# Kernel tuning notes

Measured on AMD Instinct MI355X. Metric: run time of the kernel, lower is better.

## Reference

```python
import jax, jax.numpy as jnp
import numpy as np

N_BATCH = 50000   # nodes being aggregated (rows of mask)
N_UNIQUE = 100000 # unique neighbor nodes (cols of mask / rows of features)
K = 16            # sampled neighbors per node
HID = 256
POOL = 128


def setup_inputs() -> dict:
    key = jax.random.key(0)
    k1, k2, k3 = jax.random.split(key, 3)
    neigh_idx = jax.random.randint(k1, (N_BATCH, K), 0, N_UNIQUE, dtype=jnp.int64)
    features = jax.random.normal(k2, (N_UNIQUE, HID), dtype=jnp.float32)
    # pool_layer weight, nn.Linear(hid, pool, bias=False): shape [pool, hid]
    W = jax.random.normal(k3, (POOL, HID), dtype=jnp.float32) * (1.0 / np.sqrt(HID))
    return {"neigh_idx": neigh_idx, "features": features, "W": W}


def reference(neigh_idx, features, W):
    # pool_feats = pool_layer(features): [M, POOL]
    pool_feats = jnp.einsum("mh,ph->mp", features, W)
    # mean over sampled neighbors, equivalent to (mask / num_neigh) @ pool_feats
    # without materializing the dense [N, M] mask.
    to_feats = jnp.mean(pool_feats[neigh_idx], axis=1)  # [N, POOL]
    return to_feats
```

## Files before the change

kernel.cpp:

```cpp
#include <hip/hip_runtime.h>


#define N_NODES  50000
#define N_UNIQUE 100000
#define KNEI     16
#define HID      256
#define POOL     128

#define NBLOCKS  512
#define NPB      ((N_NODES + NBLOCKS - 1) / NBLOCKS)

__global__ __launch_bounds__(256) void fused_meanpool_kernel(
    const int*   __restrict__ idx,
    const float* __restrict__ feats,
    const float* __restrict__ W,
    float* __restrict__ out)
{
    __shared__ float  mf[HID];
    __shared__ float4 part[8][32];

    const int tid = threadIdx.x;
    const int og  = tid & 31;
    const int ksl = tid >> 5;

    float4 w[4][8];
#pragma unroll
    for (int e = 0; e < 4; ++e) {
        const float* wr = W + (size_t)(og * 4 + e) * HID + ksl * 32;
#pragma unroll
        for (int j4 = 0; j4 < 8; ++j4)
            w[e][j4] = *reinterpret_cast<const float4*>(wr + j4 * 4);
    }

    const int node0 = blockIdx.x * NPB;
    for (int i = 0; i < NPB; ++i) {
        const int node = node0 + i;
        if (node >= N_NODES) break;

        const int* ip = idx + node * KNEI;
        float v = 0.f;
#pragma unroll
        for (int k = 0; k < KNEI; ++k) {
            int r = ip[k];
            r = ((unsigned)r < (unsigned)N_UNIQUE) ? r : 0;
            v += feats[(size_t)r * HID + tid];
        }
        mf[tid] = v;
        __syncthreads();

        float4 acc = make_float4(0.f, 0.f, 0.f, 0.f);
        const float4* mfp = reinterpret_cast<const float4*>(&mf[ksl * 32]);
#pragma unroll
        for (int j4 = 0; j4 < 8; ++j4) {
            const float4 m4 = mfp[j4];
            acc.x = fmaf(w[0][j4].x, m4.x, acc.x);
            acc.x = fmaf(w[0][j4].y, m4.y, acc.x);
            acc.x = fmaf(w[0][j4].z, m4.z, acc.x);
            acc.x = fmaf(w[0][j4].w, m4.w, acc.x);
            acc.y = fmaf(w[1][j4].x, m4.x, acc.y);
            acc.y = fmaf(w[1][j4].y, m4.y, acc.y);
            acc.y = fmaf(w[1][j4].z, m4.z, acc.y);
            acc.y = fmaf(w[1][j4].w, m4.w, acc.y);
            acc.z = fmaf(w[2][j4].x, m4.x, acc.z);
            acc.z = fmaf(w[2][j4].y, m4.y, acc.z);
            acc.z = fmaf(w[2][j4].z, m4.z, acc.z);
            acc.z = fmaf(w[2][j4].w, m4.w, acc.z);
            acc.w = fmaf(w[3][j4].x, m4.x, acc.w);
            acc.w = fmaf(w[3][j4].y, m4.y, acc.w);
            acc.w = fmaf(w[3][j4].z, m4.z, acc.w);
            acc.w = fmaf(w[3][j4].w, m4.w, acc.w);
        }
        part[ksl][og] = acc;
        __syncthreads();

        if (tid < 32) {
            float4 s = part[0][tid];
#pragma unroll
            for (int k = 1; k < 8; ++k) {
                const float4 p4 = part[k][tid];
                s.x += p4.x; s.y += p4.y; s.z += p4.z; s.w += p4.w;
            }
            const float inv = 1.f / (float)KNEI;
            s.x *= inv; s.y *= inv; s.z *= inv; s.w *= inv;
            *reinterpret_cast<float4*>(out + (size_t)node * POOL + tid * 4) = s;
        }
    }
}

extern "C" void kernel_launch(void* const* d_in, const int* in_sizes, int n_in,
                              void* d_out, int out_size, void* d_ws, size_t ws_size,
                              hipStream_t stream) {
    const int*   idx   = (const int*)d_in[0];
    const float* feats = (const float*)d_in[1];
    const float* W     = (const float*)d_in[2];
    float* out = (float*)d_out;

    fused_meanpool_kernel<<<NBLOCKS, 256, 0, stream>>>(idx, feats, W, out);
}
```

Baseline: 287.6 us.

## Stage indices in LDS, gather neighbor rows as float4 per wave, more blocks

Indices for all nodes in a block are preloaded into shared memory once. Each wavefront now gathers 4 neighbor rows with float4 loads instead of every thread doing 16 scalar loads. Partial sums go through shared memory and are reduced inside the matvec. The grid grows from 512 to 2000 blocks, which is meant to raise memory-level parallelism and occupancy, at the cost of more W register reloads per block and an extra LDS reduction.

```diff
diff --git a/kernel.cpp b/kernel.cpp
--- a/kernel.cpp
+++ b/kernel.cpp
@@ -7,8 +7,8 @@
 #define HID      256
 #define POOL     128
 
-#define NBLOCKS  512
-#define NPB      ((N_NODES + NBLOCKS - 1) / NBLOCKS)
+#define NBLOCKS  2000
+#define NPB      25
 
 __global__ __launch_bounds__(256) void fused_meanpool_kernel(
     const int*   __restrict__ idx,
@@ -16,12 +16,15 @@
     const float* __restrict__ W,
     float* __restrict__ out)
 {
-    __shared__ float  mf[HID];
-    __shared__ float4 part[8][32];
+    __shared__ float4 part1[4][64];
+    __shared__ float4 part2[8][32];
+    __shared__ int    idxc[NPB * KNEI];
 
-    const int tid = threadIdx.x;
-    const int og  = tid & 31;
-    const int ksl = tid >> 5;
+    const int tid  = threadIdx.x;
+    const int wv   = tid >> 6;
+    const int lane = tid & 63;
+    const int og   = tid & 31;
+    const int ksl  = tid >> 5;
 
     float4 w[4][8];
 #pragma unroll
@@ -33,26 +36,44 @@
     }
 
     const int node0 = blockIdx.x * NPB;
+
+    for (int j = tid; j < NPB * KNEI; j += 256) {
+        int v = idx[node0 * KNEI + j];
+        idxc[j] = ((unsigned)v < (unsigned)N_UNIQUE) ? v : 0;
+    }
+    __syncthreads();
+
     for (int i = 0; i < NPB; ++i) {
-        const int node = node0 + i;
-        if (node >= N_NODES) break;
-
-        const int* ip = idx + node * KNEI;
-        float v = 0.f;
-#pragma unroll
-        for (int k = 0; k < KNEI; ++k) {
-            int r = ip[k];
-            r = ((unsigned)r < (unsigned)N_UNIQUE) ? r : 0;
-            v += feats[(size_t)r * HID + tid];
-        }
-        mf[tid] = v;
+        const int kb = i * KNEI + wv * 4;
+        const int r0 = idxc[kb + 0];
+        const int r1 = idxc[kb + 1];
+        const int r2 = idxc[kb + 2];
+        const int r3 = idxc[kb + 3];
+        const float4 v0 = reinterpret_cast<const float4*>(feats + (size_t)r0 * HID)[lane];
+        const float4 v1 = reinterpret_cast<const float4*>(feats + (size_t)r1 * HID)[lane];
+        const float4 v2 = reinterpret_cast<const float4*>(feats + (size_t)r2 * HID)[lane];
+        const float4 v3 = reinterpret_cast<const float4*>(feats + (size_t)r3 * HID)[lane];
+        float4 s;
+        s.x = (v0.x + v1.x) + (v2.x + v3.x);
+        s.y = (v0.y + v1.y) + (v2.y + v3.y);
+        s.z = (v0.z + v1.z) + (v2.z + v3.z);
+        s.w = (v0.w + v1.w) + (v2.w + v3.w);
+        part1[wv][lane] = s;
         __syncthreads();
 
         float4 acc = make_float4(0.f, 0.f, 0.f, 0.f);
-        const float4* mfp = reinterpret_cast<const float4*>(&mf[ksl * 32]);
 #pragma unroll
         for (int j4 = 0; j4 < 8; ++j4) {
-            const float4 m4 = mfp[j4];
+            const int fi = ksl * 8 + j4;
+            const float4 a0 = part1[0][fi];
+            const float4 a1 = part1[1][fi];
+            const float4 a2 = part1[2][fi];
+            const float4 a3 = part1[3][fi];
+            float4 m4;
+            m4.x = (a0.x + a1.x) + (a2.x + a3.x);
+            m4.y = (a0.y + a1.y) + (a2.y + a3.y);
+            m4.z = (a0.z + a1.z) + (a2.z + a3.z);
+            m4.w = (a0.w + a1.w) + (a2.w + a3.w);
             acc.x = fmaf(w[0][j4].x, m4.x, acc.x);
             acc.x = fmaf(w[0][j4].y, m4.y, acc.x);
             acc.x = fmaf(w[0][j4].z, m4.z, acc.x);
@@ -70,19 +91,19 @@
             acc.w = fmaf(w[3][j4].z, m4.z, acc.w);
             acc.w = fmaf(w[3][j4].w, m4.w, acc.w);
         }
-        part[ksl][og] = acc;
+        part2[ksl][og] = acc;
         __syncthreads();
 
         if (tid < 32) {
-            float4 s = part[0][tid];
+            float4 s3 = part2[0][tid];
 #pragma unroll
             for (int k = 1; k < 8; ++k) {
-                const float4 p4 = part[k][tid];
-                s.x += p4.x; s.y += p4.y; s.z += p4.z; s.w += p4.w;
+                const float4 p4 = part2[k][tid];
+                s3.x += p4.x; s3.y += p4.y; s3.z += p4.z; s3.w += p4.w;
             }
             const float inv = 1.f / (float)KNEI;
-            s.x *= inv; s.y *= inv; s.z *= inv; s.w *= inv;
-            *reinterpret_cast<float4*>(out + (size_t)node * POOL + tid * 4) = s;
+            s3.x *= inv; s3.y *= inv; s3.z *= inv; s3.w *= inv;
+            *reinterpret_cast<float4*>(out + (size_t)(node0 + i) * POOL + tid * 4) = s3;
         }
     }
 }
```

After: 315.0 us. 9.5% more time.

## Process four nodes per pass with float4 gathers and transposed W from cache

Applied to the files above, without the earlier changes.

Replaces the per-node loop with passes that handle four nodes at once. Each wavefront gathers one node's 16 neighbor rows as float4 loads and tree-reduces them. Neighbor indices are staged in shared memory, and W is transposed by a separate pre-kernel so the projection streams it from L1/L2 instead of keeping it in registers. Block count rises and occupancy is hinted at 4 blocks per CU. The cost is an extra kernel launch and repeated W reads from cache, in exchange for more memory-level parallelism on the gather.

```diff
diff --git a/kernel.cpp b/kernel.cpp
--- a/kernel.cpp
+++ b/kernel.cpp
@@ -7,82 +7,114 @@
 #define HID      256
 #define POOL     128
 
-#define NBLOCKS  512
-#define NPB      ((N_NODES + NBLOCKS - 1) / NBLOCKS)
+#define NBLOCKS  2084
+#define NPB      24
+#define PASSES   6
 
-__global__ __launch_bounds__(256) void fused_meanpool_kernel(
+__global__ __launch_bounds__(256) void transpose_W_kernel(
+    const float* __restrict__ W, float* __restrict__ Wt)
+{
+    int t = blockIdx.x * 256 + threadIdx.x;
+    if (t < POOL * HID) {
+        int h = t >> 7;
+        int p = t & 127;
+        Wt[t] = W[p * HID + h];
+    }
+}
+
+__global__ __launch_bounds__(256, 4) void fused_meanpool_kernel(
     const int*   __restrict__ idx,
     const float* __restrict__ feats,
-    const float* __restrict__ W,
+    const float* __restrict__ Wt,
     float* __restrict__ out)
 {
-    __shared__ float  mf[HID];
-    __shared__ float4 part[8][32];
+    __shared__ float4 mf4[4 * 64];
+    __shared__ float4 part2[8][4][32];
+    __shared__ int    idxc[NPB * KNEI];
 
-    const int tid = threadIdx.x;
-    const int og  = tid & 31;
-    const int ksl = tid >> 5;
-
-    float4 w[4][8];
-#pragma unroll
-    for (int e = 0; e < 4; ++e) {
-        const float* wr = W + (size_t)(og * 4 + e) * HID + ksl * 32;
-#pragma unroll
-        for (int j4 = 0; j4 < 8; ++j4)
-            w[e][j4] = *reinterpret_cast<const float4*>(wr + j4 * 4);
-    }
+    const int tid  = threadIdx.x;
+    const int wv   = tid >> 6;
+    const int lane = tid & 63;
+    const int og   = tid & 31;
+    const int ksl  = tid >> 5;
 
     const int node0 = blockIdx.x * NPB;
-    for (int i = 0; i < NPB; ++i) {
-        const int node = node0 + i;
-        if (node >= N_NODES) break;
 
-        const int* ip = idx + node * KNEI;
-        float v = 0.f;
+    for (int j = tid; j < NPB * KNEI; j += 256) {
+        int gj = node0 * KNEI + j;
+        int v  = (gj < N_NODES * KNEI) ? idx[gj] : 0;
+        idxc[j] = ((unsigned)v < (unsigned)N_UNIQUE) ? v : 0;
+    }
+    __syncthreads();
+
+    const float4* feats4 = reinterpret_cast<const float4*>(feats);
+    const float4* Wt4    = reinterpret_cast<const float4*>(Wt);
+
+    for (int pass = 0; pass < PASSES; ++pass) {
+        {
+            const int ib = pass * 64 + wv * 16;
+            float4 t[KNEI];
 #pragma unroll
-        for (int k = 0; k < KNEI; ++k) {
-            int r = ip[k];
-            r = ((unsigned)r < (unsigned)N_UNIQUE) ? r : 0;
-            v += feats[(size_t)r * HID + tid];
+            for (int k = 0; k < KNEI; ++k)
+                t[k] = feats4[(size_t)idxc[ib + k] * 64 + lane];
+#pragma unroll
+            for (int s = 8; s >= 1; s >>= 1)
+#pragma unroll
+                for (int k = 0; k < s; ++k) {
+                    t[k].x += t[k + s].x; t[k].y += t[k + s].y;
+                    t[k].z += t[k + s].z; t[k].w += t[k + s].w;
+                }
+            mf4[wv * 64 + lane] = t[0];
         }
-        mf[tid] = v;
         __syncthreads();
 
-        float4 acc = make_float4(0.f, 0.f, 0.f, 0.f);
-        const float4* mfp = reinterpret_cast<const float4*>(&mf[ksl * 32]);
+        float4 acc0 = {0,0,0,0}, acc1 = {0,0,0,0}, acc2 = {0,0,0,0}, acc3 = {0,0,0,0};
 #pragma unroll
         for (int j4 = 0; j4 < 8; ++j4) {
-            const float4 m4 = mfp[j4];
-            acc.x = fmaf(w[0][j4].x, m4.x, acc.x);
-            acc.x = fmaf(w[0][j4].y, m4.y, acc.x);
-            acc.x = fmaf(w[0][j4].z, m4.z, acc.x);
-            acc.x = fmaf(w[0][j4].w, m4.w, acc.x);
-            acc.y = fmaf(w[1][j4].x, m4.x, acc.y);
-            acc.y = fmaf(w[1][j4].y, m4.y, acc.y);
-            acc.y = fmaf(w[1][j4].z, m4.z, acc.y);
-            acc.y = fmaf(w[1][j4].w, m4.w, acc.y);
-            acc.z = fmaf(w[2][j4].x, m4.x, acc.z);
-            acc.z = fmaf(w[2][j4].y, m4.y, acc.z);
-            acc.z = fmaf(w[2][j4].z, m4.z, acc.z);
-            acc.z = fmaf(w[2][j4].w, m4.w, acc.z);
-            acc.w = fmaf(w[3][j4].x, m4.x, acc.w);
-            acc.w = fmaf(w[3][j4].y, m4.y, acc.w);
-            acc.w = fmaf(w[3][j4].z, m4.z, acc.w);
-            acc.w = fmaf(w[3][j4].w, m4.w, acc.w);
+            float4 wt[4];
+#pragma unroll
+            for (int c = 0; c < 4; ++c)
+                wt[c] = Wt4[(size_t)(ksl * 32 + j4 * 4 + c) * 32 + og];
+            const float4 m0 = mf4[0 * 64 + ksl * 8 + j4];
+            const float4 m1 = mf4[1 * 64 + ksl * 8 + j4];
+            const float4 m2 = mf4[2 * 64 + ksl * 8 + j4];
+            const float4 m3 = mf4[3 * 64 + ksl * 8 + j4];
+#define PROJ(A, M)                                                  \
+            A.x = fmaf(wt[0].x, M.x, A.x); A.x = fmaf(wt[1].x, M.y, A.x); \
+            A.x = fmaf(wt[2].x, M.z, A.x); A.x = fmaf(wt[3].x, M.w, A.x); \
+            A.y = fmaf(wt[0].y, M.x, A.y); A.y = fmaf(wt[1].y, M.y, A.y); \
+            A.y = fmaf(wt[2].y, M.z, A.y); A.y = fmaf(wt[3].y, M.w, A.y); \
+            A.z = fmaf(wt[0].z, M.x, A.z); A.z = fmaf(wt[1].z, M.y, A.z); \
+            A.z = fmaf(wt[2].z, M.z, A.z); A.z = fmaf(wt[3].z, M.w, A.z); \
+            A.w = fmaf(wt[0].w, M.x, A.w); A.w = fmaf(wt[1].w, M.y, A.w); \
+            A.w = fmaf(wt[2].w, M.z, A.w); A.w = fmaf(wt[3].w, M.w, A.w);
+            PROJ(acc0, m0)
+            PROJ(acc1, m1)
+            PROJ(acc2, m2)
+            PROJ(acc3, m3)
+#undef PROJ
         }
-        part[ksl][og] = acc;
+        part2[ksl][0][og] = acc0;
+        part2[ksl][1][og] = acc1;
+        part2[ksl][2][og] = acc2;
+        part2[ksl][3][og] = acc3;
         __syncthreads();
 
-        if (tid < 32) {
-            float4 s = part[0][tid];
+        if (tid < 128) {
+            const int n = tid >> 5;
+            const int o = tid & 31;
+            float4 s = part2[0][n][o];
 #pragma unroll
             for (int k = 1; k < 8; ++k) {
-                const float4 p4 = part[k][tid];
+                const float4 p4 = part2[k][n][o];
                 s.x += p4.x; s.y += p4.y; s.z += p4.z; s.w += p4.w;
             }
-            const float inv = 1.f / (float)KNEI;
-            s.x *= inv; s.y *= inv; s.z *= inv; s.w *= inv;
-            *reinterpret_cast<float4*>(out + (size_t)node * POOL + tid * 4) = s;
+            const int node = node0 + pass * 4 + n;
+            if (node < N_NODES) {
+                const float inv = 1.f / (float)KNEI;
+                s.x *= inv; s.y *= inv; s.z *= inv; s.w *= inv;
+                *reinterpret_cast<float4*>(out + (size_t)node * POOL + o * 4) = s;
+            }
         }
     }
 }
@@ -94,6 +126,8 @@
     const float* feats = (const float*)d_in[1];
     const float* W     = (const float*)d_in[2];
     float* out = (float*)d_out;
+    float* Wt  = (float*)d_ws;
 
-    fused_meanpool_kernel<<<NBLOCKS, 256, 0, stream>>>(idx, feats, W, out);
+    transpose_W_kernel<<<(POOL * HID + 255) / 256, 256, 0, stream>>>(W, Wt);
+    fused_meanpool_kernel<<<NBLOCKS, 256, 0, stream>>>(idx, feats, Wt, out);
 }
```

New measurement: 662.1 us. 2.3x slower.

## Process four nodes per pass with 512-thread blocks and staged indices

Applied to the files above, without the earlier changes.

Replaces the one-node-per-iteration loop with 512-thread blocks that gather four nodes per pass. Each thread loads 16 features into independent registers and sums them as a tree, which raises memory-level parallelism. All neighbor indices for a block are preloaded into shared memory once. The W slice held per thread is halved so one loaded weight register can serve four nodes' matvecs. This cuts barriers per node and puts more gathers in flight, at the cost of more shared memory, a 16-way partial reduction, and hardcoded sizes (2500×20 must equal N_NODES exactly).

```diff
diff --git a/kernel.cpp b/kernel.cpp
--- a/kernel.cpp
+++ b/kernel.cpp
@@ -7,82 +7,110 @@
 #define HID      256
 #define POOL     128
 
-#define NBLOCKS  512
-#define NPB      ((N_NODES + NBLOCKS - 1) / NBLOCKS)
+#define NBLOCKS  2500
+#define NPB      20
+#define PASSES   5
 
-__global__ __launch_bounds__(256) void fused_meanpool_kernel(
+__global__ __launch_bounds__(512) void fused_meanpool_kernel(
     const int*   __restrict__ idx,
     const float* __restrict__ feats,
     const float* __restrict__ W,
     float* __restrict__ out)
 {
-    __shared__ float  mf[HID];
-    __shared__ float4 part[8][32];
+    __shared__ float  mf[4][HID];
+    __shared__ float4 part2[16][4][32];
+    __shared__ int    idxc[NPB * KNEI];
 
     const int tid = threadIdx.x;
     const int og  = tid & 31;
-    const int ksl = tid >> 5;
+    const int ksl = (tid >> 5) & 15;
+    const int ch  = tid & 255;
+    const int sub = tid >> 8;
 
-    float4 w[4][8];
+    float4 w[4][4];
 #pragma unroll
     for (int e = 0; e < 4; ++e) {
-        const float* wr = W + (size_t)(og * 4 + e) * HID + ksl * 32;
+        const float* wr = W + (size_t)(og * 4 + e) * HID + ksl * 16;
 #pragma unroll
-        for (int j4 = 0; j4 < 8; ++j4)
+        for (int j4 = 0; j4 < 4; ++j4)
             w[e][j4] = *reinterpret_cast<const float4*>(wr + j4 * 4);
     }
+#pragma unroll
+    for (int e = 0; e < 4; ++e)
+#pragma unroll
+        for (int j4 = 0; j4 < 4; ++j4)
+            asm volatile("" : "+v"(w[e][j4].x), "+v"(w[e][j4].y),
+                              "+v"(w[e][j4].z), "+v"(w[e][j4].w));
 
     const int node0 = blockIdx.x * NPB;
-    for (int i = 0; i < NPB; ++i) {
-        const int node = node0 + i;
-        if (node >= N_NODES) break;
 
-        const int* ip = idx + node * KNEI;
-        float v = 0.f;
+    for (int j = tid; j < NPB * KNEI; j += 512) {
+        int v = idx[node0 * KNEI + j];
+        idxc[j] = ((unsigned)v < (unsigned)N_UNIQUE) ? v : 0;
+    }
+    __syncthreads();
+
+    for (int pass = 0; pass < PASSES; ++pass) {
 #pragma unroll
-        for (int k = 0; k < KNEI; ++k) {
-            int r = ip[k];
-            r = ((unsigned)r < (unsigned)N_UNIQUE) ? r : 0;
-            v += feats[(size_t)r * HID + tid];
+        for (int j = 0; j < 2; ++j) {
+            const int n = j * 2 + sub;
+            const int* ip = idxc + (pass * 4 + n) * KNEI;
+            float t[KNEI];
+#pragma unroll
+            for (int k = 0; k < KNEI; ++k)
+                t[k] = feats[(size_t)ip[k] * HID + ch];
+#pragma unroll
+            for (int s = 8; s >= 1; s >>= 1)
+#pragma unroll
+                for (int k = 0; k < s; ++k) t[k] += t[k + s];
+            mf[n][ch] = t[0];
         }
-        mf[tid] = v;
         __syncthreads();
 
-        float4 acc = make_float4(0.f, 0.f, 0.f, 0.f);
-        const float4* mfp = reinterpret_cast<const float4*>(&mf[ksl * 32]);
+        float4 acc[4];
 #pragma unroll
-        for (int j4 = 0; j4 < 8; ++j4) {
-            const float4 m4 = mfp[j4];
-            acc.x = fmaf(w[0][j4].x, m4.x, acc.x);
-            acc.x = fmaf(w[0][j4].y, m4.y, acc.x);
-            acc.x = fmaf(w[0][j4].z, m4.z, acc.x);
-            acc.x = fmaf(w[0][j4].w, m4.w, acc.x);
-            acc.y = fmaf(w[1][j4].x, m4.x, acc.y);
-            acc.y = fmaf(w[1][j4].y, m4.y, acc.y);
-            acc.y = fmaf(w[1][j4].z, m4.z, acc.y);
-            acc.y = fmaf(w[1][j4].w, m4.w, acc.y);
-            acc.z = fmaf(w[2][j4].x, m4.x, acc.z);
-            acc.z = fmaf(w[2][j4].y, m4.y, acc.z);
-            acc.z = fmaf(w[2][j4].z, m4.z, acc.z);
-            acc.z = fmaf(w[2][j4].w, m4.w, acc.z);
-            acc.w = fmaf(w[3][j4].x, m4.x, acc.w);
-            acc.w = fmaf(w[3][j4].y, m4.y, acc.w);
-            acc.w = fmaf(w[3][j4].z, m4.z, acc.w);
-            acc.w = fmaf(w[3][j4].w, m4.w, acc.w);
+        for (int n = 0; n < 4; ++n) acc[n] = make_float4(0.f, 0.f, 0.f, 0.f);
+#pragma unroll
+        for (int j4 = 0; j4 < 4; ++j4) {
+#pragma unroll
+            for (int n = 0; n < 4; ++n) {
+                const float4 m4 =
+                    *reinterpret_cast<const float4*>(&mf[n][ksl * 16 + j4 * 4]);
+                acc[n].x = fmaf(w[0][j4].x, m4.x, acc[n].x);
+                acc[n].x = fmaf(w[0][j4].y, m4.y, acc[n].x);
+                acc[n].x = fmaf(w[0][j4].z, m4.z, acc[n].x);
+                acc[n].x = fmaf(w[0][j4].w, m4.w, acc[n].x);
+                acc[n].y = fmaf(w[1][j4].x, m4.x, acc[n].y);
+                acc[n].y = fmaf(w[1][j4].y, m4.y, acc[n].y);
+                acc[n].y = fmaf(w[1][j4].z, m4.z, acc[n].y);
+                acc[n].y = fmaf(w[1][j4].w, m4.w, acc[n].y);
+                acc[n].z = fmaf(w[2][j4].x, m4.x, acc[n].z);
+                acc[n].z = fmaf(w[2][j4].y, m4.y, acc[n].z);
+                acc[n].z = fmaf(w[2][j4].z, m4.z, acc[n].z);
+                acc[n].z = fmaf(w[2][j4].w, m4.w, acc[n].z);
+                acc[n].w = fmaf(w[3][j4].x, m4.x, acc[n].w);
+                acc[n].w = fmaf(w[3][j4].y, m4.y, acc[n].w);
+                acc[n].w = fmaf(w[3][j4].z, m4.z, acc[n].w);
+                acc[n].w = fmaf(w[3][j4].w, m4.w, acc[n].w);
+            }
         }
-        part[ksl][og] = acc;
+#pragma unroll
+        for (int n = 0; n < 4; ++n) part2[ksl][n][og] = acc[n];
         __syncthreads();
 
-        if (tid < 32) {
-            float4 s = part[0][tid];
+        if (tid < 128) {
+            const int n = tid >> 5;
+            const int o = tid & 31;
+            float4 s = part2[0][n][o];
 #pragma unroll
-            for (int k = 1; k < 8; ++k) {
-                const float4 p4 = part[k][tid];
+            for (int k = 1; k < 16; ++k) {
+                const float4 p4 = part2[k][n][o];
                 s.x += p4.x; s.y += p4.y; s.z += p4.z; s.w += p4.w;
             }
             const float inv = 1.f / (float)KNEI;
             s.x *= inv; s.y *= inv; s.z *= inv; s.w *= inv;
-            *reinterpret_cast<float4*>(out + (size_t)node * POOL + tid * 4) = s;
+            const int node = node0 + pass * 4 + n;
+            *reinterpret_cast<float4*>(out + (size_t)node * POOL + o * 4) = s;
         }
     }
 }
@@ -95,5 +123,5 @@
     const float* W     = (const float*)d_in[2];
     float* out = (float*)d_out;
 
-    fused_meanpool_kernel<<<NBLOCKS, 256, 0, stream>>>(idx, feats, W, out);
+    fused_meanpool_kernel<<<NBLOCKS, 512, 0, stream>>>(idx, feats, W, out);
 }
```

Result: slower. 297.8 us (+3.5%).
